# Optimization experiments

Measured on AMD Instinct MI355X. Metric: run time of the kernel, lower is better.

Reference implementation:

```python
import jax, jax.numpy as jnp
import numpy as np

EPS = 1e-5
KH = 8   # chunk size used in torch.split -> head_dim
DH = 8   # number of heads = D // KH; also the sqrt scale in the source


def fc(x, W, b, g, be):
    # 1x1 conv == linear over last dim, then BatchNorm2d (training-mode batch
    # stats over all dims except channel), then ReLU.
    y = jnp.einsum('btnd,de->btne', x, W) + b
    mu = jnp.mean(y, axis=(0, 1, 2))
    var = jnp.var(y, axis=(0, 1, 2))
    return jax.nn.relu(g * (y - mu) * jax.lax.rsqrt(var + EPS) + be)


def split_heads(x):
    # torch.cat(torch.split(x, KH, dim=-1), dim=0): chunks of size KH -> stacked on batch
    B, T, N, D = x.shape
    d = D // KH
    return jnp.moveaxis(x.reshape(B, T, N, d, KH), 3, 0).reshape(d * B, T, N, KH)


def merge_heads(x, B):
    dB, T, N, Kh = x.shape
    d = dB // B
    return jnp.moveaxis(x.reshape(d, B, T, N, Kh), 0, 3).reshape(B, T, N, d * Kh)


def setup_inputs() -> dict:
    key = jax.random.key(0)
    ks = jax.random.split(key, 16)
    B, T, N, D = 8, 12, 512, 64
    s = 1.0 / np.sqrt(D)
    inp = {
        'Q': jax.random.normal(ks[0], (B, T, N, D), jnp.float32),
        'Kin': jax.random.normal(ks[1], (B, T, N, D), jnp.float32),
        'mask': jax.random.randint(ks[2], (B, T, N, D), 0, 2).astype(jnp.float32),
        'batch_size': B,
        'Wq': jax.random.normal(ks[3], (D, D), jnp.float32) * s,
        'bq': jnp.zeros((D,), jnp.float32),
        'gq': jnp.ones((D,), jnp.float32),
        'betaq': jnp.zeros((D,), jnp.float32),
        'Wk': jax.random.normal(ks[4], (D, D), jnp.float32) * s,
        'bk': jnp.zeros((D,), jnp.float32),
        'gk': jnp.ones((D,), jnp.float32),
        'betak': jnp.zeros((D,), jnp.float32),
        'Wv': jax.random.normal(ks[5], (D, D), jnp.float32) * s,
        'bv': jnp.zeros((D,), jnp.float32),
        'gv': jnp.ones((D,), jnp.float32),
        'betav': jnp.zeros((D,), jnp.float32),
        'Wo': jax.random.normal(ks[6], (D, D), jnp.float32) * s,
        'bo': jnp.zeros((D,), jnp.float32),
        'go': jnp.ones((D,), jnp.float32),
        'betao': jnp.zeros((D,), jnp.float32),
    }
    return inp


def reference(Q, Kin, mask, batch_size, Wq, bq, gq, betaq, Wk, bk, gk, betak,
              Wv, bv, gv, betav, Wo, bo, go, betao):
    q = split_heads(fc(Q, Wq, bq, gq, betaq))      # [d*B, T, N, KH]
    k = split_heads(fc(Kin, Wk, bk, gk, betak))
    v = split_heads(fc(Kin, Wv, bv, gv, betav))
    m = split_heads(mask)
    # mask.shape == query.shape branch: mask @ ones(key)^T -> row-sum broadcast
    # over key axis; masked_fill where that product == 0.
    mrow = jnp.sum(m, axis=-1, keepdims=True)      # [d*B, T, N, 1]
    scores = jnp.einsum('btnk,btmk->btnm', q, k) / jnp.sqrt(jnp.float32(DH))
    scores = jnp.where(mrow == 0.0, jnp.float32(-1e9), scores)
    attn = jax.nn.softmax(scores, axis=-1)
    out = jnp.einsum('btnm,btmk->btnk', attn, v)
    out = merge_heads(out, batch_size)             # [B, T, N, D]
    return fc(out, Wo, bo, go, betao)
```

## Files before the change

kernel.cpp:

```cpp
#include <hip/hip_runtime.h>
#include <hip/hip_bf16.h>

#define RTOT 49152
#define RT9  442368
#define EPSF 1e-5f
#define SCQ 0.5101062398836783f

typedef _Float16 h2 __attribute__((ext_vector_type(2)));
typedef _Float16 half8 __attribute__((ext_vector_type(8)));
typedef float f32x16 __attribute__((ext_vector_type(16)));

__device__ __forceinline__ h2 cvt2h(float a, float b) {
    return __builtin_bit_cast(h2, __builtin_amdgcn_cvt_pkrtz(a, b));
}
__device__ __forceinline__ unsigned int bcu(h2 v) { return __builtin_bit_cast(unsigned int, v); }

__device__ __forceinline__ void swap32(unsigned int& x, unsigned int& y, int hi) {
#if __has_builtin(__builtin_amdgcn_permlane32_swap)
    auto r = __builtin_amdgcn_permlane32_swap(x, y, false, false);
    x = r[0]; y = r[1];
#else
    unsigned int xs = (unsigned int)__shfl_xor((int)x, 32, 64);
    unsigned int ys = (unsigned int)__shfl_xor((int)y, 32, 64);
    unsigned int nx = hi ? ys : x;
    unsigned int ny = hi ? y : xs;
    x = nx; y = ny;
#endif
}

__device__ __forceinline__ half8 ldaf(const float* __restrict__ X, size_t base) {
    const float4* p = (const float4*)(X + base);
    float4 x = p[0], y = p[1];
    uint4 u = make_uint4(bcu(cvt2h(x.x, x.y)), bcu(cvt2h(x.z, x.w)),
                         bcu(cvt2h(y.x, y.y)), bcu(cvt2h(y.z, y.w)));
    return __builtin_bit_cast(half8, u);
}
__device__ __forceinline__ half8 ldbf(const char* WT, int e, int k0) {
    int off = ((e * 64 + k0) * 2) ^ ((e & 7) << 4);
    return *(const half8*)(WT + off);
}

__global__ __launch_bounds__(512) void gemm_qkv(
        const float* __restrict__ Qin, const float* __restrict__ Kin,
        const float* __restrict__ mask,
        const float* __restrict__ Wq, const float* __restrict__ bq,
        const float* __restrict__ Wk, const float* __restrict__ bk,
        const float* __restrict__ Wv, const float* __restrict__ bv,
        _Float16* __restrict__ Yq, _Float16* __restrict__ Yk,
        _Float16* __restrict__ Vr, _Float16* __restrict__ zt,
        float* __restrict__ stats) {
    __shared__ char WT[8192];
    __shared__ _Float16 YT[256 * 72];
    __shared__ float red[128];
    int tid = threadIdx.x;
    int which = blockIdx.y;
    const float* X    = which ? Kin : Qin;
    const float* W    = which == 0 ? Wq : (which == 1 ? Wk : Wv);
    const float* bias = which == 0 ? bq : (which == 1 ? bk : bv);
    float* st = stats + which * 128;

#pragma unroll
    for (int j = 0; j < 8; j++) {
        int i = j * 512 + tid;
        int d = i >> 6, e = i & 63;
        int off = ((e * 64 + d) * 2) ^ ((e & 7) << 4);
        *(_Float16*)(&WT[off]) = (_Float16)W[i];
    }
    if (tid < 128) red[tid] = 0.f;

    int wvi = tid >> 6, lane = tid & 63, ln = lane & 31, hi = lane >> 5;
    int row = blockIdx.x * 256 + wvi * 32 + ln;

    half8 af[4];
#pragma unroll
    for (int kc = 0; kc < 4; kc++)
        af[kc] = ldaf(X, (size_t)row * 64 + kc * 16 + 8 * hi);

    if ((int)(blockIdx.x % 3) == which && tid < 256) {
        int mrow = blockIdx.x * 256 + tid;
        const float4* mr = (const float4*)(mask + (size_t)mrow * 64);
        float s[8];
#pragma unroll
        for (int h8 = 0; h8 < 8; h8++) s[h8] = 0.f;
#pragma unroll
        for (int i = 0; i < 16; i++) {
            float4 m = mr[i];
            s[i >> 1] += m.x + m.y + m.z + m.w;
        }
#pragma unroll
        for (int h8 = 0; h8 < 8; h8++)
            zt[(size_t)h8 * RTOT + mrow] = (_Float16)((s[h8] == 0.f) ? 0.f : SCQ);
    }
    __syncthreads();

    f32x16 acc[2];
#pragma unroll
    for (int ct = 0; ct < 2; ct++) {
#pragma unroll
        for (int r = 0; r < 16; r++) acc[ct][r] = 0.f;
        int e = ct * 32 + ln;
#pragma unroll
        for (int kc = 0; kc < 4; kc++) {
            half8 bf = ldbf(WT, e, kc * 16 + 8 * hi);
            acc[ct] = __builtin_amdgcn_mfma_f32_32x32x16_f16(af[kc], bf, acc[ct], 0, 0, 0);
        }
    }

#pragma unroll
    for (int ct = 0; ct < 2; ct++) {
        int cc = ct * 32 + ln;
        float bv_ = bias[cc];
        float s = 0.f, q = 0.f;
#pragma unroll
        for (int r = 0; r < 16; r++) {
            float v = acc[ct][r] + bv_;
            s += v; q += v * v;
            int lrow = wvi * 32 + (r & 3) + 8 * (r >> 2) + 4 * hi;
            YT[lrow * 72 + cc] = (_Float16)v;
        }
        s += __shfl_xor(s, 32, 64);
        q += __shfl_xor(q, 32, 64);
        if (lane < 32) {
            atomicAdd(&red[cc], s);
            atomicAdd(&red[64 + cc], q);
        }
    }
    __syncthreads();
    if (tid < 128) atomicAdd(&st[tid], red[tid]);

    if (which < 2) {
        _Float16* Y = which == 0 ? Yq : Yk;
#pragma unroll
        for (int j = 0; j < 4; j++) {
            int idx = j * 512 + tid;
            int h = idx >> 8, r = idx & 255;
            half8 v = *(const half8*)&YT[r * 72 + h * 8];
            *(half8*)(Y + ((size_t)h * RTOT + blockIdx.x * 256 + r) * 8) = v;
        }
    } else {
        int chBase = blockIdx.x * 32;
#pragma unroll
        for (int j = 0; j < 4; j++) {
            int idx = j * 512 + tid;
            int h = idx >> 8, rem = idx & 255;
            int ch = rem >> 3, c = rem & 7;
            half8 w;
#pragma unroll
            for (int i = 0; i < 8; i++)
                w[i] = YT[(ch * 8 + i) * 72 + h * 8 + c];
            *(half8*)(Vr + (size_t)h * RT9 + (size_t)(chBase + ch) * 72 + c * 8) = w;
        }
        if (tid < 256) {
            int h = tid >> 5, ch = tid & 31;
            half8 one8;
#pragma unroll
            for (int i = 0; i < 8; i++) one8[i] = (_Float16)1.0f;
            *(half8*)(Vr + (size_t)h * RT9 + (size_t)(chBase + ch) * 72 + 64) = one8;
        }
    }
}

__global__ __launch_bounds__(512) void attn_mfma(
        const _Float16* __restrict__ Yq, const _Float16* __restrict__ Yk,
        const _Float16* __restrict__ Vr, const _Float16* __restrict__ zt,
        const float* __restrict__ stats,
        const float* __restrict__ gq, const float* __restrict__ betaq,
        const float* __restrict__ gk, const float* __restrict__ betak,
        const float* __restrict__ gv, const float* __restrict__ betav,
        _Float16* __restrict__ O) {
    __shared__ __align__(16) _Float16 KL[4096];
    __shared__ __align__(16) _Float16 VS[4608];
    __shared__ __align__(16) _Float16 OL[4096];
    __shared__ float CF2[48];

    int p = blockIdx.x;
    int h = p / 96;
    int bt = p - h * 96;
    int row0 = bt * 512;
    int co = h * 8;
    int tid = threadIdx.x;

    if (tid < 24) {
        int s = tid >> 3, c7 = tid & 7;
        int c = co + c7;
        const float* g  = s == 0 ? gq : (s == 1 ? gk : gv);
        const float* be = s == 0 ? betaq : (s == 1 ? betak : betav);
        const float* stp = stats + s * 128;
        float inv = 1.f / (float)RTOT;
        float mean = stp[c] * inv;
        float var  = stp[64 + c] * inv - mean * mean;
        float a = g[c] * rsqrtf(var + EPSF);
        CF2[s * 16 + c7] = a;
        CF2[s * 16 + 8 + c7] = be[c] - mean * a;
    }

    int wv = tid >> 6;
    int lane = tid & 63;
    int ln = lane & 31;
    int hi = lane >> 5;

    const _Float16* Ykh = Yk + ((size_t)h * RTOT + row0) * 8;
    const _Float16* Vrh = Vr + (size_t)h * RT9 + (size_t)(row0 >> 3) * 72;
    const _Float16* Yqh = Yq + ((size_t)h * RTOT + row0) * 8;

    half8 yqs[2];
    float zms[2];
    if (!hi) {
#pragma unroll
        for (int s = 0; s < 2; s++) {
            int n0 = (wv + 8 * s) * 32;
            yqs[s] = *(const half8*)(Yqh + (n0 + ln) * 8);
            zms[s] = (float)zt[(size_t)h * RTOT + row0 + n0 + ln];
        }
    }
    half8 yk = *(const half8*)(Ykh + tid * 8);
    half8 vv0 = ((const half8*)Vrh)[tid];
    half8 vv1;
    if (tid < 64) vv1 = ((const half8*)Vrh)[512 + tid];
    __syncthreads();

    {
        half8 kv;
#pragma unroll
        for (int c = 0; c < 8; c++)
            kv[c] = (_Float16)fmaxf(CF2[16 + c] * (float)yk[c] + CF2[24 + c], 0.f);
        *(half8*)&KL[tid * 8] = kv;
    }
    {
        int c = tid % 9;
        if (c < 8) {
            float a = CF2[32 + c], b = CF2[40 + c];
#pragma unroll
            for (int e = 0; e < 8; e++)
                vv0[e] = (_Float16)fmaxf(a * (float)vv0[e] + b, 0.f);
        }
        ((half8*)VS)[tid] = vv0;
        if (tid < 64) {
            int c1 = (512 + tid) % 9;
            if (c1 < 8) {
                float a = CF2[32 + c1], b = CF2[40 + c1];
#pragma unroll
                for (int e = 0; e < 8; e++)
                    vv1[e] = (_Float16)fmaxf(a * (float)vv1[e] + b, 0.f);
            }
            ((half8*)VS)[512 + tid] = vv1;
        }
    }
    __syncthreads();

    f32x16 m12;
#pragma unroll
    for (int r = 0; r < 16; r++) m12[r] = -12.f;
    half8 hzero;
#pragma unroll
    for (int i = 0; i < 8; i++) hzero[i] = (_Float16)0.f;

    half8 qf0 = hzero, qf1 = hzero;
    if (!hi) {
#pragma unroll
        for (int c = 0; c < 8; c++) {
            qf0[c] = (_Float16)(fmaxf(CF2[c] * (float)yqs[0][c] + CF2[8 + c], 0.f) * zms[0]);
            qf1[c] = (_Float16)(fmaxf(CF2[c] * (float)yqs[1][c] + CF2[8 + c], 0.f) * zms[1]);
        }
    }

    f32x16 acc0, acc1;
#pragma unroll
    for (int r = 0; r < 16; r++) { acc0[r] = 0.f; acc1[r] = 0.f; }

#pragma unroll 2
    for (int t = 0; t < 16; t++) {
        half8 kf = hzero;
        if (!hi) kf = *(const half8*)&KL[(t * 32 + ln) * 8];
        f32x16 sv0 = __builtin_amdgcn_mfma_f32_32x32x16_f16(kf, qf0, m12, 0, 0, 0);
        f32x16 sv1 = __builtin_amdgcn_mfma_f32_32x32x16_f16(kf, qf1, m12, 0, 0, 0);
        float pe0[16], pe1[16];
#pragma unroll
        for (int r = 0; r < 16; r++) {
            pe0[r] = __builtin_amdgcn_exp2f(sv0[r]);
            pe1[r] = __builtin_amdgcn_exp2f(sv1[r]);
        }
#pragma unroll
        for (int ks = 0; ks < 2; ks++) {
            unsigned int a1 = bcu(cvt2h(pe0[8*ks+0], pe0[8*ks+1]));
            unsigned int a2 = bcu(cvt2h(pe0[8*ks+2], pe0[8*ks+3]));
            unsigned int a3 = bcu(cvt2h(pe0[8*ks+4], pe0[8*ks+5]));
            unsigned int a4 = bcu(cvt2h(pe0[8*ks+6], pe0[8*ks+7]));
            swap32(a1, a3, hi);
            swap32(a2, a4, hi);
            half8 pa0 = __builtin_bit_cast(half8, make_uint4(a1, a2, a3, a4));
            unsigned int b1 = bcu(cvt2h(pe1[8*ks+0], pe1[8*ks+1]));
            unsigned int b2 = bcu(cvt2h(pe1[8*ks+2], pe1[8*ks+3]));
            unsigned int b3 = bcu(cvt2h(pe1[8*ks+4], pe1[8*ks+5]));
            unsigned int b4 = bcu(cvt2h(pe1[8*ks+6], pe1[8*ks+7]));
            swap32(b1, b3, hi);
            swap32(b2, b4, hi);
            half8 pa1 = __builtin_bit_cast(half8, make_uint4(b1, b2, b3, b4));
            int chunk = t * 4 + ks * 2 + hi;
            half8 vf = hzero;
            if (ln <= 8) vf = *(const half8*)&VS[chunk * 72 + ln * 8];
            acc0 = __builtin_amdgcn_mfma_f32_32x32x16_f16(pa0, vf, acc0, 0, 0, 0);
            acc1 = __builtin_amdgcn_mfma_f32_32x32x16_f16(pa1, vf, acc1, 0, 0, 0);
        }
    }

#pragma unroll
    for (int sstep = 0; sstep < 2; sstep++) {
        int n0 = (wv + 8 * sstep) * 32;
        const f32x16& acc = sstep ? acc1 : acc0;
#pragma unroll
        for (int r = 0; r < 16; r++) {
            float av = acc[r];
            float den = __shfl(av, 8 + 32 * hi, 64);
            float ov = av * __builtin_amdgcn_rcpf(den);
            if (ln < 8) {
                int nrow = n0 + (r & 3) + 8 * (r >> 2) + 4 * hi;
                OL[nrow * 8 + ln] = (_Float16)ov;
            }
        }
    }
    __syncthreads();
    ((uint4*)(O + ((size_t)h * RTOT + row0) * 8))[tid] = ((const uint4*)OL)[tid];
}

__global__ __launch_bounds__(512) void gemm_o(
        const _Float16* __restrict__ X,
        const float* __restrict__ Wo, const float* __restrict__ bo,
        _Float16* __restrict__ Yo, float* __restrict__ st) {
    __shared__ char WT[8192];
    __shared__ _Float16 YT[256 * 72];
    __shared__ float red[128];
    int tid = threadIdx.x;
#pragma unroll
    for (int j = 0; j < 8; j++) {
        int i = j * 512 + tid;
        int d = i >> 6, e = i & 63;
        int off = ((e * 64 + d) * 2) ^ ((e & 7) << 4);
        *(_Float16*)(&WT[off]) = (_Float16)Wo[i];
    }
    if (tid < 128) red[tid] = 0.f;

    int wvi = tid >> 6, lane = tid & 63, ln = lane & 31, hi = lane >> 5;
    int rowBase = blockIdx.x * 256 + wvi * 32;

    half8 af[4];
#pragma unroll
    for (int kc = 0; kc < 4; kc++)
        af[kc] = *(const half8*)(X + ((size_t)(2*kc + hi) * RTOT + rowBase + ln) * 8);
    __syncthreads();

    f32x16 acc[2];
#pragma unroll
    for (int ct = 0; ct < 2; ct++) {
#pragma unroll
        for (int r = 0; r < 16; r++) acc[ct][r] = 0.f;
        int e = ct * 32 + ln;
#pragma unroll
        for (int kc = 0; kc < 4; kc++) {
            half8 bf = ldbf(WT, e, kc * 16 + 8 * hi);
            acc[ct] = __builtin_amdgcn_mfma_f32_32x32x16_f16(af[kc], bf, acc[ct], 0, 0, 0);
        }
    }

#pragma unroll
    for (int ct = 0; ct < 2; ct++) {
        int cc = ct * 32 + ln;
        float bv_ = bo[cc];
        float s = 0.f, q = 0.f;
#pragma unroll
        for (int r = 0; r < 16; r++) {
            float v = acc[ct][r] + bv_;
            s += v; q += v * v;
            int lrow = wvi * 32 + (r & 3) + 8 * (r >> 2) + 4 * hi;
            YT[lrow * 72 + cc] = (_Float16)v;
        }
        s += __shfl_xor(s, 32, 64);
        q += __shfl_xor(q, 32, 64);
        if (lane < 32) {
            atomicAdd(&red[cc], s);
            atomicAdd(&red[64 + cc], q);
        }
    }
    __syncthreads();
    if (tid < 128) atomicAdd(&st[tid], red[tid]);

#pragma unroll
    for (int j = 0; j < 4; j++) {
        int idx = j * 512 + tid;
        int r = idx >> 3, c8 = idx & 7;
        half8 v = *(const half8*)&YT[r * 72 + c8 * 8];
        *(half8*)(Yo + ((size_t)(blockIdx.x * 256 + r) * 64 + c8 * 8)) = v;
    }
}

__global__ __launch_bounds__(256) void norm_relu16(const _Float16* __restrict__ Y,
                                                   const float* __restrict__ st,
                                                   const float* __restrict__ g,
                                                   const float* __restrict__ be,
                                                   float* __restrict__ out) {
    __shared__ float CF[128];
    int tid = threadIdx.x;
    if (tid < 64) {
        float inv = 1.f / (float)RTOT;
        float mean = st[tid] * inv;
        float var  = st[64 + tid] * inv - mean * mean;
        float a = g[tid] * rsqrtf(var + EPSF);
        CF[tid] = a;
        CF[64 + tid] = be[tid] - mean * a;
    }
    __syncthreads();
    int i = blockIdx.x * 256 + tid;
    half8 y = ((const half8*)Y)[i];
    int cb = (i & 7) * 8;
    float4 o0, o1;
    o0.x = fmaxf(CF[cb+0]*(float)y[0] + CF[64+cb+0], 0.f);
    o0.y = fmaxf(CF[cb+1]*(float)y[1] + CF[64+cb+1], 0.f);
    o0.z = fmaxf(CF[cb+2]*(float)y[2] + CF[64+cb+2], 0.f);
    o0.w = fmaxf(CF[cb+3]*(float)y[3] + CF[64+cb+3], 0.f);
    o1.x = fmaxf(CF[cb+4]*(float)y[4] + CF[64+cb+4], 0.f);
    o1.y = fmaxf(CF[cb+5]*(float)y[5] + CF[64+cb+5], 0.f);
    o1.z = fmaxf(CF[cb+6]*(float)y[6] + CF[64+cb+6], 0.f);
    o1.w = fmaxf(CF[cb+7]*(float)y[7] + CF[64+cb+7], 0.f);
    ((float4*)out)[2*i]   = o0;
    ((float4*)out)[2*i+1] = o1;
}

extern "C" void kernel_launch(void* const* d_in, const int* in_sizes, int n_in,
                              void* d_out, int out_size, void* d_ws, size_t ws_size,
                              hipStream_t stream) {
    const float* Q    = (const float*)d_in[0];
    const float* Kin  = (const float*)d_in[1];
    const float* mask = (const float*)d_in[2];
    const float* Wq = (const float*)d_in[4];
    const float* bq = (const float*)d_in[5];
    const float* gq = (const float*)d_in[6];
    const float* betaq = (const float*)d_in[7];
    const float* Wk = (const float*)d_in[8];
    const float* bk = (const float*)d_in[9];
    const float* gk = (const float*)d_in[10];
    const float* betak = (const float*)d_in[11];
    const float* Wv = (const float*)d_in[12];
    const float* bv = (const float*)d_in[13];
    const float* gv = (const float*)d_in[14];
    const float* betav = (const float*)d_in[15];
    const float* Wo = (const float*)d_in[16];
    const float* bo = (const float*)d_in[17];
    const float* go = (const float*)d_in[18];
    const float* betao = (const float*)d_in[19];

    const size_t TSZ = (size_t)RTOT * 64;
    _Float16* Yq = (_Float16*)d_ws;
    _Float16* Yk = Yq + TSZ;
    _Float16* Vr = Yk + TSZ;
    _Float16* Ob = Vr + (size_t)RTOT * 72;
    _Float16* Yo = Ob + TSZ;
    _Float16* zt = Yo + TSZ;
    float* stats = (float*)(zt + (size_t)8 * RTOT);

    (void)hipMemsetAsync(stats, 0, 512 * sizeof(float), stream);

    dim3 gqkv(192, 3);
    gemm_qkv<<<gqkv, 512, 0, stream>>>(Q, Kin, mask, Wq, bq, Wk, bk, Wv, bv,
                                       Yq, Yk, Vr, zt, stats);

    attn_mfma<<<768, 512, 0, stream>>>(Yq, Yk, Vr, zt, stats,
                                       gq, betaq, gk, betak, gv, betav, Ob);

    gemm_o<<<192, 512, 0, stream>>>(Ob, Wo, bo, Yo, stats + 384);

    norm_relu16<<<1536, 256, 0, stream>>>(Yo, stats + 384, go, betao, (float*)d_out);
}
```

Measured before the change: 76.38 us.

## Replace global stat atomics and memset with per-block partials reduced in attention

The QKV GEMM now writes its per-block BatchNorm partial sums to a separate buffer instead of doing global atomicAdds, and zeroes the output-stage stats in-kernel, which lets the hipMemsetAsync launch be dropped. Each attention block then reduces the 192 partials for its 8 channels itself before computing the normalization coefficients. This removes the memset launch and contention on global atomics. In exchange, every one of the 768 attention blocks repeats the partial reduction, adding global reads and an extra barrier. Zeroing stats_o inside gemm_qkv relies on gemm_qkv completing before gemm_o starts, which the stream order provides.

Measured after the change: 74.72 us, median of 3. 1.02x faster.

```diff
diff --git a/kernel.cpp b/kernel.cpp
--- a/kernel.cpp
+++ b/kernel.cpp
@@ -48,7 +48,7 @@
         const float* __restrict__ Wv, const float* __restrict__ bv,
         _Float16* __restrict__ Yq, _Float16* __restrict__ Yk,
         _Float16* __restrict__ Vr, _Float16* __restrict__ zt,
-        float* __restrict__ stats) {
+        float* __restrict__ sp1, float* __restrict__ stats_o) {
     __shared__ char WT[8192];
     __shared__ _Float16 YT[256 * 72];
     __shared__ float red[128];
@@ -57,7 +57,6 @@
     const float* X    = which ? Kin : Qin;
     const float* W    = which == 0 ? Wq : (which == 1 ? Wk : Wv);
     const float* bias = which == 0 ? bq : (which == 1 ? bk : bv);
-    float* st = stats + which * 128;
 
 #pragma unroll
     for (int j = 0; j < 8; j++) {
@@ -67,6 +66,8 @@
         *(_Float16*)(&WT[off]) = (_Float16)W[i];
     }
     if (tid < 128) red[tid] = 0.f;
+    if (blockIdx.x == 0 && which == 0 && tid < 128)
+        stats_o[tid] = 0.f;
 
     int wvi = tid >> 6, lane = tid & 63, ln = lane & 31, hi = lane >> 5;
     int row = blockIdx.x * 256 + wvi * 32 + ln;
@@ -126,7 +127,8 @@
         }
     }
     __syncthreads();
-    if (tid < 128) atomicAdd(&st[tid], red[tid]);
+    if (tid < 128)
+        sp1[((size_t)which * 192 + blockIdx.x) * 128 + tid] = red[tid];
 
     if (which < 2) {
         _Float16* Y = which == 0 ? Yq : Yk;
@@ -163,7 +165,7 @@
 __global__ __launch_bounds__(512) void attn_mfma(
         const _Float16* __restrict__ Yq, const _Float16* __restrict__ Yk,
         const _Float16* __restrict__ Vr, const _Float16* __restrict__ zt,
-        const float* __restrict__ stats,
+        const float* __restrict__ sp1,
         const float* __restrict__ gq, const float* __restrict__ betaq,
         const float* __restrict__ gk, const float* __restrict__ betak,
         const float* __restrict__ gv, const float* __restrict__ betav,
@@ -171,6 +173,7 @@
     __shared__ __align__(16) _Float16 KL[4096];
     __shared__ __align__(16) _Float16 VS[4608];
     __shared__ __align__(16) _Float16 OL[4096];
+    __shared__ float SR[48];
     __shared__ float CF2[48];
 
     int p = blockIdx.x;
@@ -180,20 +183,6 @@
     int co = h * 8;
     int tid = threadIdx.x;
 
-    if (tid < 24) {
-        int s = tid >> 3, c7 = tid & 7;
-        int c = co + c7;
-        const float* g  = s == 0 ? gq : (s == 1 ? gk : gv);
-        const float* be = s == 0 ? betaq : (s == 1 ? betak : betav);
-        const float* stp = stats + s * 128;
-        float inv = 1.f / (float)RTOT;
-        float mean = stp[c] * inv;
-        float var  = stp[64 + c] * inv - mean * mean;
-        float a = g[c] * rsqrtf(var + EPSF);
-        CF2[s * 16 + c7] = a;
-        CF2[s * 16 + 8 + c7] = be[c] - mean * a;
-    }
-
     int wv = tid >> 6;
     int lane = tid & 63;
     int ln = lane & 31;
@@ -217,6 +206,34 @@
     half8 vv0 = ((const half8*)Vrh)[tid];
     half8 vv1;
     if (tid < 64) vv1 = ((const half8*)Vrh)[512 + tid];
+
+    if (tid < 384) {
+        int v = tid >> 3;
+        int part = tid & 7;
+        int s = v >> 4, i16 = v & 15;
+        int ci = (i16 < 8) ? (co + i16) : (64 + co + (i16 - 8));
+        const float* base = sp1 + ((size_t)s * 192 + part * 24) * 128 + ci;
+        float a = 0.f;
+#pragma unroll
+        for (int b = 0; b < 24; b++)
+            a += base[b * 128];
+        a += __shfl_xor(a, 1, 64);
+        a += __shfl_xor(a, 2, 64);
+        a += __shfl_xor(a, 4, 64);
+        if (part == 0) SR[v] = a;
+    }
+    __syncthreads();
+    if (tid < 24) {
+        int s = tid >> 3, c7 = tid & 7;
+        const float* g  = s == 0 ? gq : (s == 1 ? gk : gv);
+        const float* be = s == 0 ? betaq : (s == 1 ? betak : betav);
+        float inv = 1.f / (float)RTOT;
+        float mean = SR[s * 16 + c7] * inv;
+        float var  = SR[s * 16 + 8 + c7] * inv - mean * mean;
+        float a = g[co + c7] * rsqrtf(var + EPSF);
+        CF2[s * 16 + c7] = a;
+        CF2[s * 16 + 8 + c7] = be[co + c7] - mean * a;
+    }
     __syncthreads();
 
     {
@@ -455,18 +472,17 @@
     _Float16* Ob = Vr + (size_t)RTOT * 72;
     _Float16* Yo = Ob + TSZ;
     _Float16* zt = Yo + TSZ;
-    float* stats = (float*)(zt + (size_t)8 * RTOT);
-
-    (void)hipMemsetAsync(stats, 0, 512 * sizeof(float), stream);
+    float* sp1 = (float*)(zt + (size_t)8 * RTOT);
+    float* stats_o = sp1 + 3 * 192 * 128;
 
     dim3 gqkv(192, 3);
     gemm_qkv<<<gqkv, 512, 0, stream>>>(Q, Kin, mask, Wq, bq, Wk, bk, Wv, bv,
-                                       Yq, Yk, Vr, zt, stats);
-
-    attn_mfma<<<768, 512, 0, stream>>>(Yq, Yk, Vr, zt, stats,
+                                       Yq, Yk, Vr, zt, sp1, stats_o);
+
+    attn_mfma<<<768, 512, 0, stream>>>(Yq, Yk, Vr, zt, sp1,
                                        gq, betaq, gk, betak, gv, betav, Ob);
 
-    gemm_o<<<192, 512, 0, stream>>>(Ob, Wo, bo, Yo, stats + 384);
-
-    norm_relu16<<<1536, 256, 0, stream>>>(Yo, stats + 384, go, betao, (float*)d_out);
-}
+    gemm_o<<<192, 512, 0, stream>>>(Ob, Wo, bo, Yo, stats_o);
+
+    norm_relu16<<<1536, 256, 0, stream>>>(Yo, stats_o, go, betao, (float*)d_out);
+}
```
